# Kernel tuning notes

Hardware: AMD Instinct MI355X
Metric: run time of the kernel (lower is better)

Reference implementation:

```python
import jax, jax.numpy as jnp
import numpy as np

DEGREE = 3  # B-spline degree (cubic)


def bspline_basis(x, knots, degree):
    """Cox-de Boor B-spline basis evaluation.
    x: (..., ) values; knots: (K,) non-decreasing knot vector.
    Returns (..., K - degree - 1) basis values.
    """
    xb = x[..., None]
    # degree-0: indicator of half-open knot spans
    B = ((xb >= knots[:-1]) & (xb < knots[1:])).astype(x.dtype)
    # include x == last knot in the final span (standard clamped-spline convention)
    B = B.at[..., -1].set(jnp.where(x == knots[-1], jnp.ones_like(x), B[..., -1]))
    for d in range(1, degree + 1):
        ld = knots[d:-1] - knots[:-(d + 1)]          # left denominators
        rd = knots[d + 1:] - knots[1:-d]             # right denominators
        lterm = jnp.where(ld > 0, (xb - knots[:-(d + 1)]) / jnp.where(ld > 0, ld, 1.0), 0.0) * B[..., :-1]
        rterm = jnp.where(rd > 0, (knots[d + 1:] - xb) / jnp.where(rd > 0, rd, 1.0), 0.0) * B[..., 1:]
        B = lterm + rterm
    return B


def setup_inputs() -> dict:
    key = jax.random.key(0)
    k1, k2, k3 = jax.random.split(key, 3)
    in_feat, out_feat, num_knots, degree = 512, 512, 64, DEGREE
    batch = 2048
    grid_min, grid_max = -1.0, 1.0
    # inputs within grid range so spline bases are active
    x = jax.random.uniform(k1, (batch, in_feat), jnp.float32, grid_min, grid_max)
    # coeffs ~ 0.1 * randn, matching torch init
    coeffs = 0.1 * jax.random.normal(k2, (in_feat, out_feat, num_knots - degree - 1), jnp.float32)
    # xavier-uniform base_weights
    bound = float(np.sqrt(6.0 / (in_feat + out_feat)))
    base_weights = jax.random.uniform(k3, (in_feat, out_feat), jnp.float32, -bound, bound)
    # clamped uniform knot vector: (degree+1) repeats at ends + 56 interior points
    left = jnp.full((degree + 1,), grid_min, jnp.float32)
    right = jnp.full((degree + 1,), grid_max, jnp.float32)
    internal = jnp.linspace(grid_min, grid_max, num_knots - 2 * (degree + 1) + 2, dtype=jnp.float32)[1:-1]
    knots = jnp.concatenate([left, internal, right])
    return {"x": x, "coeffs": coeffs, "base_weights": base_weights, "knots": knots}


def reference(x, coeffs, base_weights, knots):
    # basis: (batch, in_feat, n_basis) -- computed ONCE per input feature
    basis = bspline_basis(x, knots, DEGREE)
    # spline term: sum_j sum_k coeffs[j,o,k] * B_k(x[:,j])
    spline = jnp.einsum('bjk,jok->bo', basis, coeffs)
    # base term: sum_j base_weights[j,o] * SiLU(x[:,j])
    base = jax.nn.silu(x) @ base_weights
    return spline + base
```

## Files before the change

kernel.cpp:

```cpp
#include <hip/hip_runtime.h>
#include <hip/hip_bf16.h>
#include <stdint.h>

#define BATCH 2048
#define INF   512
#define OUTF  512
#define NB    60
#define KP    64
#define LDK   128

typedef float    f32x4 __attribute__((ext_vector_type(4)));
typedef unsigned u32x4 __attribute__((ext_vector_type(4)));

__device__ __forceinline__ unsigned short f2bf(float f) {
  unsigned u = __builtin_bit_cast(unsigned, f);
  u += 0x7fff + ((u >> 16) & 1);
  return (unsigned short)(u >> 16);
}

__device__ __forceinline__ void gll16(const void* g, void* l) {
  __builtin_amdgcn_global_load_lds(
      (const __attribute__((address_space(1))) void*)g,
      (__attribute__((address_space(3))) void*)l, 16, 0, 0);
}

__global__ __launch_bounds__(256) void prep_ct(const float* __restrict__ coeffs,
                                               const float* __restrict__ bw,
                                               unsigned short* __restrict__ CT) {
  int tg  = blockIdx.x * 256 + threadIdx.x;
  int row = tg >> 3;
  int pos = tg & 7;
  const float* src = coeffs + (long)row * NB;
  unsigned short v[8];
  if (pos < 7) {
    float4 c0 = *(const float4*)(src + pos * 8);
    float4 c1 = *(const float4*)(src + pos * 8 + 4);
    v[0]=f2bf(c0.x); v[1]=f2bf(c0.y); v[2]=f2bf(c0.z); v[3]=f2bf(c0.w);
    v[4]=f2bf(c1.x); v[5]=f2bf(c1.y); v[6]=f2bf(c1.z); v[7]=f2bf(c1.w);
  } else {
    float4 c0 = *(const float4*)(src + 56);
    v[0]=f2bf(c0.x); v[1]=f2bf(c0.y); v[2]=f2bf(c0.z); v[3]=f2bf(c0.w);
    v[4]=f2bf(bw[row]); v[5]=0; v[6]=0; v[7]=0;
  }
  uint4 pack;
  pack.x = (unsigned)v[0] | ((unsigned)v[1] << 16);
  pack.y = (unsigned)v[2] | ((unsigned)v[3] << 16);
  pack.z = (unsigned)v[4] | ((unsigned)v[5] << 16);
  pack.w = (unsigned)v[6] | ((unsigned)v[7] << 16);
  *(uint4*)(CT + (long)row * KP + pos * 8) = pack;
}

__global__ __launch_bounds__(256) void basis_kernel(const float* __restrict__ x,
                                                    const float* __restrict__ knots,
                                                    uint4* __restrict__ recs) {
  __shared__ float xl[64][65];
  __shared__ float Uk[64];
  int t  = threadIdx.x;
  int bt = blockIdx.x & 31, jt = blockIdx.x >> 5;
  int b0 = bt * 64, j0 = jt * 64;
  if (t < 64) Uk[t] = knots[t];
  for (int it = 0; it < 16; ++it) {
    int f = it * 256 + t;
    int r = f >> 6, c = f & 63;
    xl[r][c] = x[(long)(b0 + r) * INF + j0 + c];
  }
  __syncthreads();
  int bl = t & 63;
  int jg = t >> 6;
  for (int jj = 0; jj < 16; ++jj) {
    int jl = jg * 16 + jj;
    float xv = xl[bl][jl];
    int i = (int)floorf((xv + 1.0f) * 28.5f);
    i = max(0, min(56, i));
    if (xv < Uk[i + 3]) i--;
    else if (xv >= Uk[i + 4]) i++;
    i = max(0, min(56, i));
    int m = i + 3;
    float l1 = xv - Uk[m],     r1 = Uk[m + 1] - xv;
    float l2 = xv - Uk[m - 1], r2 = Uk[m + 2] - xv;
    float l3 = xv - Uk[m - 2], r3 = Uk[m + 3] - xv;
    float N0 = 1.0f, N1, N2, N3, temp, saved;
    temp = N0 / (r1 + l1); N0 = r1 * temp; N1 = l1 * temp;
    temp = N0 / (r1 + l2); N0 = r1 * temp; saved = l2 * temp;
    temp = N1 / (r2 + l1); N1 = saved + r2 * temp; N2 = l1 * temp;
    temp = N0 / (r1 + l3); N0 = r1 * temp; saved = l3 * temp;
    temp = N1 / (r2 + l2); N1 = saved + r2 * temp; saved = l2 * temp;
    temp = N2 / (r3 + l1); N2 = saved + r3 * temp; N3 = l1 * temp;
    float sil = xv / (1.0f + __expf(-xv));
    uint4 rec;
    rec.x = (unsigned)f2bf(N0) | ((unsigned)f2bf(N1) << 16);
    rec.y = (unsigned)f2bf(N2) | ((unsigned)f2bf(N3) << 16);
    rec.z = (unsigned)f2bf(sil) | ((unsigned)i << 16);
    rec.w = 0;
    recs[(long)(j0 + jl) * BATCH + b0 + bl] = rec;
  }
}

__global__ __launch_bounds__(256, 2) void gemm_kernel(const unsigned short* __restrict__ CT,
                                                      const uint4* __restrict__ recs,
                                                      float* __restrict__ out) {
  __shared__ __align__(16) unsigned short Bl[128 * KP];
  __shared__ __align__(16) unsigned short Al[128 * KP];
  __shared__ uint4 recl[128];
  int t = threadIdx.x;
  int lane = t & 63, wid = t >> 6;
  int bx = blockIdx.x;
  int mt = bx & 15, nt = (bx >> 4) & 3, kt = bx >> 6;
  int b0 = mt * 128, o0 = nt * 128, j0 = kt * 64;
  int wr = wid >> 1, wc = wid & 1;

  f32x4 acc[4][4];
#pragma unroll
  for (int mm = 0; mm < 4; ++mm)
#pragma unroll
    for (int nn = 0; nn < 4; ++nn) { f32x4 z = {0.f, 0.f, 0.f, 0.f}; acc[mm][nn] = z; }

  for (int jj = 0; jj < 64; ++jj) {
    int j = j0 + jj;
    __syncthreads();
#pragma unroll
    for (int it = 0; it < 4; ++it) {
      int g  = it * 256 + t;
      int o  = g >> 3, ls = g & 7;
      int ks = ls ^ (o & 7);
      const unsigned short* src = CT + ((long)(j * 512 + o0 + o) << 6) + ks * 8;
      gll16(src, (char*)Bl + (it * 256 + wid * 64) * 16);
    }
    if (wid < 2)
      gll16(recs + ((long)j * BATCH + b0 + wid * 64 + lane),
            (char*)recl + wid * 64 * 16);
#pragma unroll
    for (int it = 0; it < 4; ++it)
      ((uint4*)Al)[it * 256 + t] = make_uint4(0, 0, 0, 0);
    __syncthreads();
    if (t < 128) {
      uint4 rec = recl[t];
      int r = t;
      int s = rec.z >> 16;
      unsigned short w[4] = {(unsigned short)rec.x, (unsigned short)(rec.x >> 16),
                             (unsigned short)rec.y, (unsigned short)(rec.y >> 16)};
#pragma unroll
      for (int e = 0; e < 4; ++e) {
        int k = s + e;
        int byte = r * LDK + (((k >> 3) ^ (r & 7)) << 4) + (k & 7) * 2;
        *(unsigned short*)((char*)Al + byte) = w[e];
      }
      int byte = r * LDK + ((7 ^ (r & 7)) << 4) + 8;
      *(unsigned short*)((char*)Al + byte) = (unsigned short)rec.z;
    }
    __syncthreads();
#pragma unroll
    for (int kp = 0; kp < 2; ++kp) {
      int ksl = kp * 4 + (lane >> 4);
      u32x4 av[4], bv[4];
#pragma unroll
      for (int mm = 0; mm < 4; ++mm) {
        int row = wr * 64 + mm * 16 + (lane & 15);
        av[mm] = *(const u32x4*)((const char*)Al + row * LDK + ((ksl ^ (row & 7)) << 4));
      }
#pragma unroll
      for (int nn = 0; nn < 4; ++nn) {
        int col = wc * 64 + nn * 16 + (lane & 15);
        bv[nn] = *(const u32x4*)((const char*)Bl + col * LDK + ((ksl ^ (col & 7)) << 4));
      }
#pragma unroll
      for (int mm = 0; mm < 4; ++mm)
#pragma unroll
        for (int nn = 0; nn < 4; ++nn)
          asm volatile("v_mfma_f32_16x16x32_bf16 %0, %1, %2, %0"
                       : "+v"(acc[mm][nn]) : "v"(av[mm]), "v"(bv[nn]));
    }
  }
  int r0 = (lane >> 4) * 4, c0 = lane & 15;
#pragma unroll
  for (int mm = 0; mm < 4; ++mm)
#pragma unroll
    for (int nn = 0; nn < 4; ++nn) {
      int grow = b0 + wr * 64 + mm * 16 + r0;
      int gcol = o0 + wc * 64 + nn * 16 + c0;
#pragma unroll
      for (int e = 0; e < 4; ++e)
        unsafeAtomicAdd(&out[(long)(grow + e) * OUTF + gcol], acc[mm][nn][e]);
    }
}

extern "C" void kernel_launch(void* const* d_in, const int* in_sizes, int n_in,
                              void* d_out, int out_size, void* d_ws, size_t ws_size,
                              hipStream_t stream) {
  const float* x      = (const float*)d_in[0];
  const float* coeffs = (const float*)d_in[1];
  const float* bw     = (const float*)d_in[2];
  const float* knots  = (const float*)d_in[3];
  float* out = (float*)d_out;

  const size_t CT_BYTES  = (size_t)INF * OUTF * KP * 2;
  const size_t REC_BYTES = (size_t)INF * BATCH * 16;
  if (ws_size < CT_BYTES + REC_BYTES) return;

  unsigned short* CT = (unsigned short*)d_ws;
  uint4* recs = (uint4*)((char*)d_ws + CT_BYTES);

  hipMemsetAsync(d_out, 0, (size_t)BATCH * OUTF * sizeof(float), stream);
  prep_ct<<<(INF * OUTF * 8) / 256, 256, 0, stream>>>(coeffs, bw, CT);
  basis_kernel<<<(BATCH / 64) * (INF / 64), 256, 0, stream>>>(x, knots, recs);
  gemm_kernel<<<512, 256, 0, stream>>>(CT, recs, out);
}
```

Before: 128.7 us.

## Double-buffer GEMM tiles and sparsely update basis A-tile

Gives the B (coefficient) and A (basis) tiles in the GEMM kernel two shared-memory buffers each, and prefetches the next input feature's coefficient tile and basis record while the current one is multiplied. Instead of zeroing the whole A tile every step, it clears only the four slots written two steps earlier in the same buffer and writes the new four basis values across all 256 threads. It also reorders the block index so blocks sharing an output tile are adjacent. The aim is to hide global-load latency and cut per-iteration LDS zeroing and barrier overhead. In exchange it doubles shared memory and depends on hand-placed waitcnt counts and barriers.

```diff
diff --git a/kernel.cpp b/kernel.cpp
--- a/kernel.cpp
+++ b/kernel.cpp
@@ -8,6 +8,7 @@
 #define NB    60
 #define KP    64
 #define LDK   128
+#define NJ    64
 
 typedef float    f32x4 __attribute__((ext_vector_type(4)));
 typedef unsigned u32x4 __attribute__((ext_vector_type(4)));
@@ -99,15 +100,16 @@
 __global__ __launch_bounds__(256, 2) void gemm_kernel(const unsigned short* __restrict__ CT,
                                                       const uint4* __restrict__ recs,
                                                       float* __restrict__ out) {
-  __shared__ __align__(16) unsigned short Bl[128 * KP];
-  __shared__ __align__(16) unsigned short Al[128 * KP];
-  __shared__ uint4 recl[128];
+  __shared__ __align__(16) unsigned short Bl[2][128 * KP];
+  __shared__ __align__(16) unsigned short Al[2][128 * KP];
   int t = threadIdx.x;
   int lane = t & 63, wid = t >> 6;
   int bx = blockIdx.x;
-  int mt = bx & 15, nt = (bx >> 4) & 3, kt = bx >> 6;
+  int kt = bx & 7, mt = (bx >> 3) & 15, nt = bx >> 7;
   int b0 = mt * 128, o0 = nt * 128, j0 = kt * 64;
   int wr = wid >> 1, wc = wid & 1;
+  int r  = t & 127;
+  int eh = t >> 7;
 
   f32x4 acc[4][4];
 #pragma unroll
@@ -115,62 +117,99 @@
 #pragma unroll
     for (int nn = 0; nn < 4; ++nn) { f32x4 z = {0.f, 0.f, 0.f, 0.f}; acc[mm][nn] = z; }
 
-  for (int jj = 0; jj < 64; ++jj) {
-    int j = j0 + jj;
-    __syncthreads();
-#pragma unroll
-    for (int it = 0; it < 4; ++it) {
-      int g  = it * 256 + t;
-      int o  = g >> 3, ls = g & 7;
-      int ks = ls ^ (o & 7);
-      const unsigned short* src = CT + ((long)(j * 512 + o0 + o) << 6) + ks * 8;
-      gll16(src, (char*)Bl + (it * 256 + wid * 64) * 16);
-    }
-    if (wid < 2)
-      gll16(recs + ((long)j * BATCH + b0 + wid * 64 + lane),
-            (char*)recl + wid * 64 * 16);
-#pragma unroll
-    for (int it = 0; it < 4; ++it)
-      ((uint4*)Al)[it * 256 + t] = make_uint4(0, 0, 0, 0);
-    __syncthreads();
-    if (t < 128) {
-      uint4 rec = recl[t];
-      int r = t;
-      int s = rec.z >> 16;
-      unsigned short w[4] = {(unsigned short)rec.x, (unsigned short)(rec.x >> 16),
-                             (unsigned short)rec.y, (unsigned short)(rec.y >> 16)};
-#pragma unroll
-      for (int e = 0; e < 4; ++e) {
-        int k = s + e;
-        int byte = r * LDK + (((k >> 3) ^ (r & 7)) << 4) + (k & 7) * 2;
-        *(unsigned short*)((char*)Al + byte) = w[e];
-      }
-      int byte = r * LDK + ((7 ^ (r & 7)) << 4) + 8;
-      *(unsigned short*)((char*)Al + byte) = (unsigned short)rec.z;
-    }
-    __syncthreads();
-#pragma unroll
-    for (int kp = 0; kp < 2; ++kp) {
-      int ksl = kp * 4 + (lane >> 4);
-      u32x4 av[4], bv[4];
-#pragma unroll
-      for (int mm = 0; mm < 4; ++mm) {
-        int row = wr * 64 + mm * 16 + (lane & 15);
-        av[mm] = *(const u32x4*)((const char*)Al + row * LDK + ((ksl ^ (row & 7)) << 4));
-      }
-#pragma unroll
-      for (int nn = 0; nn < 4; ++nn) {
-        int col = wc * 64 + nn * 16 + (lane & 15);
-        bv[nn] = *(const u32x4*)((const char*)Bl + col * LDK + ((ksl ^ (col & 7)) << 4));
-      }
-#pragma unroll
-      for (int mm = 0; mm < 4; ++mm)
-#pragma unroll
-        for (int nn = 0; nn < 4; ++nn)
-          asm volatile("v_mfma_f32_16x16x32_bf16 %0, %1, %2, %0"
-                       : "+v"(acc[mm][nn]) : "v"(av[mm]), "v"(bv[nn]));
-    }
-  }
+#pragma unroll
+  for (int it = 0; it < 8; ++it)
+    ((uint4*)Al)[it * 256 + t] = make_uint4(0, 0, 0, 0);
+
+#pragma unroll
+  for (int it = 0; it < 4; ++it) {
+    int g = it * 256 + t, o = g >> 3, ls = g & 7, ks = ls ^ (o & 7);
+    gll16(CT + ((long)(j0 * 512 + o0 + o) << 6) + ks * 8,
+          (char*)Bl + (it * 256 + wid * 64) * 16);
+  }
+  uint4 recA = recs[(long)j0 * BATCH + b0 + r];
+  uint4 recB;
+  int olds0 = 0, olds1 = 0;
+  asm volatile("s_waitcnt lgkmcnt(0)" ::: "memory");
+
+#define CLR(K)                                                                   \
+  if ((K) < s || (K) > s + 3)                                                    \
+    *(unsigned short*)(A + r * LDK + ((((K) >> 3) ^ (r & 7)) << 4) + ((K) & 7) * 2) = 0;
+#define PUT(K, V)                                                                \
+  *(unsigned short*)(A + r * LDK + ((((K) >> 3) ^ (r & 7)) << 4) + ((K) & 7) * 2) = (unsigned short)(V);
+
+#define BODY(CUR, JJ, RECUSE, RECLOAD, OLDS)                                     \
+  {                                                                              \
+    if ((JJ) + 1 < NJ) {                                                         \
+      int jn = j0 + (JJ) + 1;                                                    \
+      _Pragma("unroll")                                                          \
+      for (int it = 0; it < 4; ++it) {                                           \
+        int g = it * 256 + t, o = g >> 3, ls = g & 7, ks = ls ^ (o & 7);         \
+        gll16(CT + ((long)(jn * 512 + o0 + o) << 6) + ks * 8,                    \
+              (char*)Bl + (1 - (CUR)) * 16384 + (it * 256 + wid * 64) * 16);     \
+      }                                                                          \
+      RECLOAD = recs[(long)jn * BATCH + b0 + r];                                 \
+      asm volatile("s_waitcnt vmcnt(5)" ::: "memory");                           \
+    } else {                                                                     \
+      asm volatile("s_waitcnt vmcnt(0)" ::: "memory");                           \
+    }                                                                            \
+    __builtin_amdgcn_s_barrier();            \
+    {                                                                            \
+      char* A = (char*)Al + (CUR) * 16384;                                       \
+      int s = (int)(RECUSE.z >> 16);                                             \
+      if (eh == 0) {                                                             \
+        int k0 = OLDS, k1 = OLDS + 1;                                            \
+        CLR(k0) CLR(k1)                                                          \
+        PUT(s,     RECUSE.x)                                                     \
+        PUT(s + 1, RECUSE.x >> 16)                                               \
+      } else {                                                                   \
+        int k0 = OLDS + 2, k1 = OLDS + 3;                                        \
+        CLR(k0) CLR(k1)                                                          \
+        PUT(s + 2, RECUSE.y)                                                     \
+        PUT(s + 3, RECUSE.y >> 16)                                               \
+        *(unsigned short*)(A + r * LDK + ((7 ^ (r & 7)) << 4) + 8) = (unsigned short)RECUSE.z; \
+      }                                                                          \
+      OLDS = s;                                                                  \
+    }                                                                            \
+    asm volatile("s_waitcnt lgkmcnt(0)" ::: "memory");                           \
+    __builtin_amdgcn_s_barrier();                           \
+    {                                                                            \
+      const char* A = (const char*)Al + (CUR) * 16384;                           \
+      const char* B = (const char*)Bl + (CUR) * 16384;                           \
+      _Pragma("unroll")                                                          \
+      for (int kp = 0; kp < 2; ++kp) {                                           \
+        int ksl = kp * 4 + (lane >> 4);                                          \
+        u32x4 av[4], bv[4];                                                      \
+        _Pragma("unroll")                                                        \
+        for (int mm = 0; mm < 4; ++mm) {                                         \
+          int row = wr * 64 + mm * 16 + (lane & 15);                             \
+          av[mm] = *(const u32x4*)(A + row * LDK + ((ksl ^ (row & 7)) << 4));    \
+        }                                                                        \
+        _Pragma("unroll")                                                        \
+        for (int nn = 0; nn < 4; ++nn) {                                         \
+          int col = wc * 64 + nn * 16 + (lane & 15);                             \
+          bv[nn] = *(const u32x4*)(B + col * LDK + ((ksl ^ (col & 7)) << 4));    \
+        }                                                                        \
+        _Pragma("unroll")                                                        \
+        for (int mm = 0; mm < 4; ++mm)                                           \
+          _Pragma("unroll")                                                      \
+          for (int nn = 0; nn < 4; ++nn)                                         \
+            asm volatile("v_mfma_f32_16x16x32_bf16 %0, %1, %2, %0"               \
+                         : "+v"(acc[mm][nn]) : "v"(av[mm]), "v"(bv[nn]));        \
+      }                                                                          \
+    }                                                                            \
+    asm volatile("s_waitcnt lgkmcnt(0)" ::: "memory");                           \
+    __builtin_amdgcn_s_barrier();            \
+  }
+
+  for (int jt = 0; jt < 32; ++jt) {
+    BODY(0, 2 * jt,     recA, recB, olds0)
+    BODY(1, 2 * jt + 1, recB, recA, olds1)
+  }
+#undef BODY
+#undef CLR
+#undef PUT
+
   int r0 = (lane >> 4) * 4, c0 = lane & 15;
 #pragma unroll
   for (int mm = 0; mm < 4; ++mm)
```

After: 114.3 us. 1.13x faster.

## Double-buffer coefficient tiles and build sparse A fragments in registers

Applied to the files above, without the earlier changes.

The GEMM kernel now double-buffers the per-feature coefficient tile and record loads so global-to-LDS transfers for feature j+1 overlap MFMA work on feature j. The scattered LDS writes that built the sparse A tile are dropped: each lane builds its A fragment directly in registers by shifting the four packed basis values into the right K slot. The split-K factor doubles (32 features per block, 1024 blocks), occupancy is raised to 4 blocks per SM, and MFMA sections get raised wave priority. This removes two barriers and the zero-fill per step, in exchange for more atomic adds to the output and higher register and LDS pressure.

```diff
diff --git a/kernel.cpp b/kernel.cpp
--- a/kernel.cpp
+++ b/kernel.cpp
@@ -8,6 +8,7 @@
 #define NB    60
 #define KP    64
 #define LDK   128
+#define NJ    32
 
 typedef float    f32x4 __attribute__((ext_vector_type(4)));
 typedef unsigned u32x4 __attribute__((ext_vector_type(4)));
@@ -22,6 +23,21 @@
   __builtin_amdgcn_global_load_lds(
       (const __attribute__((address_space(1))) void*)g,
       (__attribute__((address_space(3))) void*)l, 16, 0, 0);
+}
+
+__device__ __forceinline__ u32x4 build_av(unsigned long long w, int s,
+                                          unsigned silu, int q) {
+  int rel = s - (q << 3);
+  int sh  = rel << 4;
+  unsigned long long lo = (rel >= 0) ? ((rel <= 3) ? (w << sh) : 0ull)
+                                     : ((rel >= -3) ? (w >> (-sh)) : 0ull);
+  unsigned long long hi = (rel >= 4) ? ((rel <= 7) ? (w << (sh - 64)) : 0ull)
+                                     : ((rel >= 1) ? (w >> (64 - sh)) : 0ull);
+  if (q == 7) hi |= (unsigned long long)silu;
+  u32x4 av;
+  av[0] = (unsigned)lo; av[1] = (unsigned)(lo >> 32);
+  av[2] = (unsigned)hi; av[3] = (unsigned)(hi >> 32);
+  return av;
 }
 
 __global__ __launch_bounds__(256) void prep_ct(const float* __restrict__ coeffs,
@@ -96,17 +112,16 @@
   }
 }
 
-__global__ __launch_bounds__(256, 2) void gemm_kernel(const unsigned short* __restrict__ CT,
+__global__ __launch_bounds__(256, 4) void gemm_kernel(const unsigned short* __restrict__ CT,
                                                       const uint4* __restrict__ recs,
                                                       float* __restrict__ out) {
-  __shared__ __align__(16) unsigned short Bl[128 * KP];
-  __shared__ __align__(16) unsigned short Al[128 * KP];
-  __shared__ uint4 recl[128];
+  __shared__ __align__(16) unsigned short Bl[2][128 * KP];
+  __shared__ __align__(16) uint4 recl[2 * 128];
   int t = threadIdx.x;
   int lane = t & 63, wid = t >> 6;
   int bx = blockIdx.x;
-  int mt = bx & 15, nt = (bx >> 4) & 3, kt = bx >> 6;
-  int b0 = mt * 128, o0 = nt * 128, j0 = kt * 64;
+  int kt = bx & 15, mt = (bx >> 4) & 15, nt = bx >> 8;
+  int b0 = mt * 128, o0 = nt * 128, j0 = kt * NJ;
   int wr = wid >> 1, wc = wid & 1;
 
   f32x4 acc[4][4];
@@ -115,62 +130,68 @@
 #pragma unroll
     for (int nn = 0; nn < 4; ++nn) { f32x4 z = {0.f, 0.f, 0.f, 0.f}; acc[mm][nn] = z; }
 
-  for (int jj = 0; jj < 64; ++jj) {
-    int j = j0 + jj;
-    __syncthreads();
-#pragma unroll
-    for (int it = 0; it < 4; ++it) {
-      int g  = it * 256 + t;
-      int o  = g >> 3, ls = g & 7;
-      int ks = ls ^ (o & 7);
-      const unsigned short* src = CT + ((long)(j * 512 + o0 + o) << 6) + ks * 8;
-      gll16(src, (char*)Bl + (it * 256 + wid * 64) * 16);
-    }
-    if (wid < 2)
-      gll16(recs + ((long)j * BATCH + b0 + wid * 64 + lane),
-            (char*)recl + wid * 64 * 16);
-#pragma unroll
-    for (int it = 0; it < 4; ++it)
-      ((uint4*)Al)[it * 256 + t] = make_uint4(0, 0, 0, 0);
-    __syncthreads();
-    if (t < 128) {
-      uint4 rec = recl[t];
-      int r = t;
-      int s = rec.z >> 16;
-      unsigned short w[4] = {(unsigned short)rec.x, (unsigned short)(rec.x >> 16),
-                             (unsigned short)rec.y, (unsigned short)(rec.y >> 16)};
-#pragma unroll
-      for (int e = 0; e < 4; ++e) {
-        int k = s + e;
-        int byte = r * LDK + (((k >> 3) ^ (r & 7)) << 4) + (k & 7) * 2;
-        *(unsigned short*)((char*)Al + byte) = w[e];
+#pragma unroll
+  for (int it = 0; it < 4; ++it) {
+    int g = it * 256 + t, o = g >> 3, ls = g & 7, ks = ls ^ (o & 7);
+    gll16(CT + ((long)(j0 * 512 + o0 + o) << 6) + ks * 8,
+          (char*)Bl + (it * 256 + wid * 64) * 16);
+  }
+  if (wid < 2)
+    gll16(recs + ((long)j0 * BATCH + b0 + wid * 64 + lane),
+          (char*)recl + wid * 64 * 16);
+  asm volatile("s_waitcnt vmcnt(0)" ::: "memory");
+  __builtin_amdgcn_s_barrier();
+
+  for (int jj = 0; jj < NJ; ++jj) {
+    int cur = jj & 1;
+    const char*  B  = (const char*)Bl + cur * 16384;
+    const uint4* RC = recl + cur * 128;
+    if (jj + 1 < NJ) {
+      int jn = j0 + jj + 1;
+#pragma unroll
+      for (int it = 0; it < 4; ++it) {
+        int g = it * 256 + t, o = g >> 3, ls = g & 7, ks = ls ^ (o & 7);
+        gll16(CT + ((long)(jn * 512 + o0 + o) << 6) + ks * 8,
+              (char*)Bl + (1 - cur) * 16384 + (it * 256 + wid * 64) * 16);
       }
-      int byte = r * LDK + ((7 ^ (r & 7)) << 4) + 8;
-      *(unsigned short*)((char*)Al + byte) = (unsigned short)rec.z;
-    }
-    __syncthreads();
+      if (wid < 2)
+        gll16(recs + ((long)jn * BATCH + b0 + wid * 64 + lane),
+              (char*)(recl + (1 - cur) * 128) + wid * 64 * 16);
+    }
+    unsigned long long w64[4]; int sS[4]; unsigned sil[4];
+#pragma unroll
+    for (int mm = 0; mm < 4; ++mm) {
+      uint4 rc = RC[wr * 64 + mm * 16 + (lane & 15)];
+      w64[mm] = ((unsigned long long)rc.y << 32) | rc.x;
+      sS[mm]  = (int)(rc.z >> 16);
+      sil[mm] = rc.z & 0xffffu;
+    }
 #pragma unroll
     for (int kp = 0; kp < 2; ++kp) {
       int ksl = kp * 4 + (lane >> 4);
-      u32x4 av[4], bv[4];
-#pragma unroll
-      for (int mm = 0; mm < 4; ++mm) {
-        int row = wr * 64 + mm * 16 + (lane & 15);
-        av[mm] = *(const u32x4*)((const char*)Al + row * LDK + ((ksl ^ (row & 7)) << 4));
-      }
+      u32x4 bv[4];
 #pragma unroll
       for (int nn = 0; nn < 4; ++nn) {
         int col = wc * 64 + nn * 16 + (lane & 15);
-        bv[nn] = *(const u32x4*)((const char*)Bl + col * LDK + ((ksl ^ (col & 7)) << 4));
+        bv[nn] = *(const u32x4*)(B + col * LDK + ((ksl ^ (col & 7)) << 4));
       }
+      u32x4 av[4];
+#pragma unroll
+      for (int mm = 0; mm < 4; ++mm)
+        av[mm] = build_av(w64[mm], sS[mm], sil[mm], ksl);
+      __builtin_amdgcn_s_setprio(1);
 #pragma unroll
       for (int mm = 0; mm < 4; ++mm)
 #pragma unroll
         for (int nn = 0; nn < 4; ++nn)
           asm volatile("v_mfma_f32_16x16x32_bf16 %0, %1, %2, %0"
                        : "+v"(acc[mm][nn]) : "v"(av[mm]), "v"(bv[nn]));
-    }
-  }
+      __builtin_amdgcn_s_setprio(0);
+    }
+    asm volatile("s_waitcnt vmcnt(0) lgkmcnt(0)" ::: "memory");
+    __builtin_amdgcn_s_barrier();
+  }
+
   int r0 = (lane >> 4) * 4, c0 = lane & 15;
 #pragma unroll
   for (int mm = 0; mm < 4; ++mm)
@@ -203,5 +224,5 @@
   hipMemsetAsync(d_out, 0, (size_t)BATCH * OUTF * sizeof(float), stream);
   prep_ct<<<(INF * OUTF * 8) / 256, 256, 0, stream>>>(coeffs, bw, CT);
   basis_kernel<<<(BATCH / 64) * (INF / 64), 256, 0, stream>>>(x, knots, recs);
-  gemm_kernel<<<512, 256, 0, stream>>>(CT, recs, out);
-}
+  gemm_kernel<<<1024, 256, 0, stream>>>(CT, recs, out);
+}
```

Result: slower. 154.9 us (+20.3%).
